# Kernel tuning notes

Measured on AMD Instinct MI355X. Metric: run time of the kernel, lower is better.

## Reference

```python
import jax, jax.numpy as jnp
import numpy as np

SAMPLE_NUM = 1024   # number of FPS centroids
RADIUS = 0.2        # ball-query radius
NEIGHBOR_NUM = 64   # max neighbors per ball


def setup_inputs() -> dict:
    key = jax.random.key(0)
    k1, k2 = jax.random.split(key)
    B, N, C = 4, 8192, 256
    xyz = jax.random.uniform(k1, (B, N, 3), dtype=jnp.float32)   # points in unit cube
    feat = jax.random.normal(k2, (B, N, C), dtype=jnp.float32)
    return {"xyz": xyz, "feat": feat}


def farthest_point_sample(xyz, K):
    """Iterative FPS. xyz: (B,N,3) -> indices (B,K). Deterministic start at index 0
    (stands in for pytorch3d's random_start_point for reproducibility)."""
    B, N, _ = xyz.shape
    start = jnp.zeros((B,), dtype=jnp.int32)
    min_d = jnp.full((B, N), jnp.inf, dtype=xyz.dtype)

    def step(carry, _):
        min_d, cur = carry
        sel = jnp.take_along_axis(xyz, cur[:, None, None], axis=1)      # (B,1,3)
        d = jnp.sum((xyz - sel) ** 2, axis=-1)                          # (B,N)
        min_d = jnp.minimum(min_d, d)
        nxt = jnp.argmax(min_d, axis=-1).astype(jnp.int32)
        return (min_d, nxt), cur

    (_, _), idxs = jax.lax.scan(step, (min_d, start), None, length=K)
    return jnp.transpose(idxs)                                          # (B,K)


def ball_query_idx(sample_xyz, xyz, radius, K):
    """For each centroid, first-K (by point index) points within radius; -1 padding.
    Matches pytorch3d ball_query index semantics."""
    B, S, _ = sample_xyz.shape
    N = xyz.shape[1]
    # squared distances via |a|^2 + |b|^2 - 2ab to avoid a (B,S,N,3) temp
    d2 = (jnp.sum(sample_xyz ** 2, -1)[:, :, None]
          + jnp.sum(xyz ** 2, -1)[:, None, :]
          - 2.0 * jnp.einsum('bsd,bnd->bsn', sample_xyz, xyz))          # (B,S,N)
    within = d2 < radius * radius
    cand = jnp.where(within, jnp.arange(N, dtype=jnp.int32), N)         # invalid -> N
    neg_topk, _ = jax.lax.top_k(-cand, K)                               # K smallest indices
    idx = -neg_topk                                                     # (B,S,K)
    return jnp.where(idx == N, -1, idx)


def reference(xyz, feat):
    B, N, C = feat.shape
    S, K = SAMPLE_NUM, NEIGHBOR_NUM
    samp_idx = farthest_point_sample(xyz, S)                            # (B,S)
    sample_xyz = jnp.take_along_axis(xyz, samp_idx[..., None], axis=1)  # (B,S,3)
    nbr_idx = ball_query_idx(sample_xyz, xyz, RADIUS, K)                # (B,S,K)
    # faithful to original gather(): -1 is replaced by idx.shape[1] == S
    idx2 = jnp.where(nbr_idx == -1, S, nbr_idx)
    neighbor_feat = jnp.take_along_axis(
        feat, idx2.reshape(B, S * K)[..., None], axis=1
    ).reshape(B, S, K, C)                                               # (B,S,K,C)
    return (sample_xyz, neighbor_feat)
```

## Files before the change

kernel.cpp:

```cpp
#include <hip/hip_runtime.h>
#include <cstdint>

#define NB   4
#define NPT  8192
#define NC   256
#define NS   1024
#define NK   64
#define FPT  16

typedef float v2f __attribute__((ext_vector_type(2)));

template <int CTRL, int RMASK>
__device__ __forceinline__ float dpp_max_step(float x) {
    const int t = __builtin_amdgcn_update_dpp(
        0, __float_as_int(x), CTRL, RMASK, 0xf, false);
    return fmaxf(x, __int_as_float(t));
}
__device__ __forceinline__ float wave_max_f32(float x) {
    x = dpp_max_step<0x111, 0xf>(x);
    x = dpp_max_step<0x112, 0xf>(x);
    x = dpp_max_step<0x114, 0xf>(x);
    x = dpp_max_step<0x118, 0xf>(x);
    x = dpp_max_step<0x142, 0xa>(x);
    x = dpp_max_step<0x143, 0xc>(x);
    return x;
}

__global__ __launch_bounds__(512) void fps_kernel(
    const float* __restrict__ xyz, float* __restrict__ sample_xyz)
{
    const int b   = blockIdx.x;
    const int tid = threadIdx.x;

    __shared__ float Xs[NPT], Ys[NPT], Zs[NPT];
    __shared__ float Samp[NS * 3];
    __shared__ unsigned long long slots[3];

    const float* base = xyz + (size_t)b * NPT * 3;

    v2f px[8], py[8], pz[8], md[8];
#pragma unroll
    for (int j = 0; j < 8; ++j) {
        const int pa = tid * FPT + j;
        const int pb = tid * FPT + 8 + j;
        const float ax = base[pa * 3 + 0], ay = base[pa * 3 + 1], az = base[pa * 3 + 2];
        const float bx = base[pb * 3 + 0], by = base[pb * 3 + 1], bz = base[pb * 3 + 2];
        px[j] = (v2f){ax, bx};
        py[j] = (v2f){ay, by};
        pz[j] = (v2f){az, bz};
        md[j] = (v2f){__builtin_inff(), __builtin_inff()};
        Xs[pa] = ax; Ys[pa] = ay; Zs[pa] = az;
        Xs[pb] = bx; Ys[pb] = by; Zs[pb] = bz;
    }
    if (tid < 3) slots[tid] = 0ull;
    __syncthreads();

    int widx = 0;
    int cur = 0, nxt = 1;
    for (int s = 0; s < NS; ++s) {
        const float sx = Xs[widx];
        const float sy = Ys[widx];
        const float sz = Zs[widx];
        if (tid == 0) {
            Samp[s * 3 + 0] = sx; Samp[s * 3 + 1] = sy; Samp[s * 3 + 2] = sz;
            slots[nxt] = 0ull;
        }

        const v2f sxv = (v2f){sx, sx};
        const v2f syv = (v2f){sy, sy};
        const v2f szv = (v2f){sz, sz};

        v2f best2 = (v2f){-1.0f, -1.0f};
        int jx = 0, jy = 0;
        {
#pragma clang fp contract(off)
#pragma unroll
            for (int j = 0; j < 8; ++j) {
                const v2f dx = px[j] - sxv;
                const v2f dy = py[j] - syv;
                const v2f dz = pz[j] - szv;
                const v2f d  = (dx * dx + dy * dy) + dz * dz;
                const v2f m  = __builtin_elementwise_min(md[j], d);
                md[j] = m;
                if (m.x > best2.x) jx = j;
                if (m.y > best2.y) jy = j;
                best2 = __builtin_elementwise_max(best2, m);
            }
        }
        float    bestval;
        unsigned bestidx;
        if (best2.y > best2.x) { bestval = best2.y; bestidx = (unsigned)(tid * FPT + 8 + jy); }
        else                   { bestval = best2.x; bestidx = (unsigned)(tid * FPT + jx); }

        const float wmax = wave_max_f32(bestval);
        const float smax = __int_as_float(
            __builtin_amdgcn_readlane(__float_as_int(wmax), 63));
        const unsigned long long msk = __ballot(bestval == smax);
        const int wl = __ffsll((long long)msk) - 1;
        const unsigned widx_w =
            (unsigned)__builtin_amdgcn_readlane((int)bestidx, wl);
        if ((tid & 63) == 0) {
            const unsigned long long key =
                ((unsigned long long)__float_as_uint(smax) << 32)
                | (unsigned long long)(0xFFFFFFFFu - widx_w);
            atomicMax(&slots[cur], key);
        }
        __syncthreads();

        const unsigned long long best = slots[cur];
        widx = (int)(0xFFFFFFFFu - (unsigned)(best & 0xFFFFFFFFull));
        cur = nxt;
        nxt = (nxt == 2) ? 0 : nxt + 1;
    }

    float* o = sample_xyz + (size_t)b * NS * 3;
    for (int i = tid; i < NS * 3; i += 512) o[i] = Samp[i];
}

__global__ __launch_bounds__(256) void bq_gather_kernel(
    const float* __restrict__ xyz, const float* __restrict__ feat,
    const float* __restrict__ sample_xyz, float* __restrict__ out_feat)
{
    const int s   = blockIdx.x;
    const int b   = blockIdx.y;
    const int tid = threadIdx.x;

    __shared__ int   list[NK];
    __shared__ int   wavecnt[4];
    __shared__ float cen[3];

    if (tid < 3) cen[tid] = sample_xyz[((size_t)b * NS + s) * 3 + tid];
    __syncthreads();
    const float sx = cen[0], sy = cen[1], sz = cen[2];
    const float na = __fadd_rn(
        __fadd_rn(__fmul_rn(sx, sx), __fmul_rn(sy, sy)), __fmul_rn(sz, sz));
    const float* bxyz = xyz + (size_t)b * NPT * 3;

    int len = 0;
    for (int c0 = 0; c0 < NPT; c0 += 256) {
        const int idx = c0 + tid;
        const float x = bxyz[idx * 3 + 0];
        const float y = bxyz[idx * 3 + 1];
        const float z = bxyz[idx * 3 + 2];
        const float nb = __fadd_rn(
            __fadd_rn(__fmul_rn(x, x), __fmul_rn(y, y)), __fmul_rn(z, z));
        const float dt = __fmaf_rn(sz, z, __fmaf_rn(sy, y, __fmul_rn(sx, x)));
        const float d2 = __fsub_rn(__fadd_rn(na, nb), __fmul_rn(2.0f, dt));
        const bool within = d2 < 0.04f;

        const unsigned long long m = __ballot(within);
        const int wv   = tid >> 6;
        const int lane = tid & 63;
        if (lane == 0) wavecnt[wv] = __popcll(m);
        __syncthreads();
        const int w0 = wavecnt[0], w1 = wavecnt[1], w2 = wavecnt[2], w3 = wavecnt[3];
        int off = len;
        if (wv > 0) off += w0;
        if (wv > 1) off += w1;
        if (wv > 2) off += w2;
        const int pre = __popcll(m & ((1ull << lane) - 1ull));
        const int pos = off + pre;
        if (within && pos < NK) list[pos] = idx;
        len += w0 + w1 + w2 + w3;
        __syncthreads();
        if (len >= NK) break;
    }
    const int llen = len < NK ? len : NK;

    const int lane = tid & 63;
    const int sub  = tid >> 6;
    const float4* fbase = (const float4*)(feat + (size_t)b * NPT * NC);
    float4* obase = (float4*)(out_feat + (((size_t)b * NS + s) * (size_t)NK) * NC);
#pragma unroll
    for (int p = 0; p < NK / 4; ++p) {
        const int k   = p * 4 + sub;
        const int row = (k < llen) ? list[k] : NS;
        const float4 v = fbase[(size_t)row * (NC / 4) + lane];
        obase[(size_t)k * (NC / 4) + lane] = v;
    }
}

extern "C" void kernel_launch(void* const* d_in, const int* in_sizes, int n_in,
                              void* d_out, int out_size, void* d_ws, size_t ws_size,
                              hipStream_t stream) {
    const float* xyz  = (const float*)d_in[0];
    const float* feat = (const float*)d_in[1];
    float* out        = (float*)d_out;
    float* sample_xyz = out;
    float* out_feat   = out + (size_t)NB * NS * 3;

    fps_kernel<<<dim3(NB), dim3(512), 0, stream>>>(xyz, sample_xyz);
    bq_gather_kernel<<<dim3(NS, NB), dim3(256), 0, stream>>>(
        xyz, feat, sample_xyz, out_feat);
}
```

Measured before the change: 886.7 us.

## Replace FPS atomicMax reduction with per-wave slots and redundant cross-wave argmax

```diff
diff --git a/kernel.cpp b/kernel.cpp
--- a/kernel.cpp
+++ b/kernel.cpp
@@ -29,12 +29,15 @@
 __global__ __launch_bounds__(512) void fps_kernel(
     const float* __restrict__ xyz, float* __restrict__ sample_xyz)
 {
-    const int b   = blockIdx.x;
-    const int tid = threadIdx.x;
-
-    __shared__ float Xs[NPT], Ys[NPT], Zs[NPT];
-    __shared__ float Samp[NS * 3];
-    __shared__ unsigned long long slots[3];
+    const int b    = blockIdx.x;
+    const int tid  = threadIdx.x;
+    const int lane = tid & 63;
+    const int wv   = tid >> 6;
+
+    __shared__ float4 Pts[NPT];
+    __shared__ float  Samp[NS * 3];
+    __shared__ float  cval[2][8];
+    __shared__ int    cidx[2][8];
 
     const float* base = xyz + (size_t)b * NPT * 3;
 
@@ -49,21 +52,36 @@
         py[j] = (v2f){ay, by};
         pz[j] = (v2f){az, bz};
         md[j] = (v2f){__builtin_inff(), __builtin_inff()};
-        Xs[pa] = ax; Ys[pa] = ay; Zs[pa] = az;
-        Xs[pb] = bx; Ys[pb] = by; Zs[pb] = bz;
-    }
-    if (tid < 3) slots[tid] = 0ull;
+        Pts[pa] = (float4){ax, ay, az, 0.0f};
+        Pts[pb] = (float4){bx, by, bz, 0.0f};
+    }
+    if (tid < 8) {
+        cval[0][tid] = (tid == 0) ? 3.0e38f : -1.0f;
+        cidx[0][tid] = 0;
+    }
     __syncthreads();
 
-    int widx = 0;
-    int cur = 0, nxt = 1;
     for (int s = 0; s < NS; ++s) {
-        const float sx = Xs[widx];
-        const float sy = Ys[widx];
-        const float sz = Zs[widx];
+        const int rb = s & 1;
+        const int wb = rb ^ 1;
+
+        const int   g  = lane & 7;
+        const float v  = cval[rb][g];
+        const int   ci = cidx[rb][g];
+        float r = v;
+        r = dpp_max_step<0x111, 0xf>(r);
+        r = dpp_max_step<0x112, 0xf>(r);
+        r = dpp_max_step<0x114, 0xf>(r);
+        const float smax = __int_as_float(
+            __builtin_amdgcn_readlane(__float_as_int(r), 7));
+        const unsigned long long mA = __ballot(v == smax);
+        const int l0   = __ffsll((long long)mA) - 1;
+        const int widx = __builtin_amdgcn_readlane(ci, l0);
+
+        const float4 cen = Pts[widx];
+        const float sx = cen.x, sy = cen.y, sz = cen.z;
         if (tid == 0) {
             Samp[s * 3 + 0] = sx; Samp[s * 3 + 1] = sy; Samp[s * 3 + 2] = sz;
-            slots[nxt] = 0ull;
         }
 
         const v2f sxv = (v2f){sx, sx};
@@ -93,24 +111,16 @@
         else                   { bestval = best2.x; bestidx = (unsigned)(tid * FPT + jx); }
 
         const float wmax = wave_max_f32(bestval);
-        const float smax = __int_as_float(
+        const float smaxw = __int_as_float(
             __builtin_amdgcn_readlane(__float_as_int(wmax), 63));
-        const unsigned long long msk = __ballot(bestval == smax);
-        const int wl = __ffsll((long long)msk) - 1;
-        const unsigned widx_w =
-            (unsigned)__builtin_amdgcn_readlane((int)bestidx, wl);
-        if ((tid & 63) == 0) {
-            const unsigned long long key =
-                ((unsigned long long)__float_as_uint(smax) << 32)
-                | (unsigned long long)(0xFFFFFFFFu - widx_w);
-            atomicMax(&slots[cur], key);
+        const unsigned long long mC = __ballot(bestval == smaxw);
+        const int wl = __ffsll((long long)mC) - 1;
+
+        if (lane == wl) {
+            cval[wb][wv] = bestval;
+            cidx[wb][wv] = (int)bestidx;
         }
         __syncthreads();
-
-        const unsigned long long best = slots[cur];
-        widx = (int)(0xFFFFFFFFu - (unsigned)(best & 0xFFFFFFFFull));
-        cur = nxt;
-        nxt = (nxt == 2) ? 0 : nxt + 1;
     }
 
     float* o = sample_xyz + (size_t)b * NS * 3;
@@ -149,15 +159,15 @@
         const bool within = d2 < 0.04f;
 
         const unsigned long long m = __ballot(within);
-        const int wv   = tid >> 6;
+        const int wvq  = tid >> 6;
         const int lane = tid & 63;
-        if (lane == 0) wavecnt[wv] = __popcll(m);
+        if (lane == 0) wavecnt[wvq] = __popcll(m);
         __syncthreads();
         const int w0 = wavecnt[0], w1 = wavecnt[1], w2 = wavecnt[2], w3 = wavecnt[3];
         int off = len;
-        if (wv > 0) off += w0;
-        if (wv > 1) off += w1;
-        if (wv > 2) off += w2;
+        if (wvq > 0) off += w0;
+        if (wvq > 1) off += w1;
+        if (wvq > 2) off += w2;
         const int pre = __popcll(m & ((1ull << lane) - 1ull));
         const int pos = off + pre;
         if (within && pos < NK) list[pos] = idx;
```

Measured after the change: 1.070 ms. 20.7% more time.
